# Kernel optimization log

Measured on AMD Instinct MI355X. Metric: run time of the kernel, lower is better.

## Reference

```python
import jax, jax.numpy as jnp
import numpy as np

B, D, C = 16384, 2048, 1000  # batch, in_features (feature dim), out_features (classes)
INIT_SCALE = 10.0
EPS = 1e-12


def setup_inputs() -> dict:
    key = jax.random.key(0)
    k1, k2 = jax.random.split(key)
    x = jax.random.normal(k1, (B, D), dtype=jnp.float32)
    weights = jax.random.normal(k2, (C, D), dtype=jnp.float32)  # prototypes
    scales = jnp.ones((1,), dtype=jnp.float32) * INIT_SCALE
    return {"x": x, "weights": weights, "scales": scales}


def reference(x, weights, scales):
    # Pairwise Euclidean distance between features [B,D] and prototypes [C,D]
    x2 = jnp.sum(x * x, axis=-1, keepdims=True)            # [B,1]
    w2 = jnp.sum(weights * weights, axis=-1)               # [C]
    cross = jnp.einsum('bd,cd->bc', x, weights)            # [B,C]
    d2 = jnp.maximum(x2 + w2[None, :] - 2.0 * cross, EPS)  # clamp for sqrt stability
    distances = jnp.sqrt(d2)                               # [B,C]
    logits = -scales * distances  # dml forward: -self.learn(distances)
    return logits
```

## Files before the change

### kernel.cpp

```cpp
#include <hip/hip_runtime.h>
#include <hip/hip_bf16.h>
#include <stdint.h>

#define B_ROWS 16384
#define D_K    2048
#define C_COLS 1000
#define C_PAD  1024
#define EPS_D2 1e-12f

typedef __attribute__((ext_vector_type(8))) short bf16x8;
typedef __attribute__((ext_vector_type(4))) float f32x4;

__device__ __forceinline__ unsigned short f2bf_rne(float f) {
    union { float f; uint32_t u; } a; a.f = f;
    uint32_t u = a.u;
    uint32_t r = (u + 0x7FFFu + ((u >> 16) & 1u)) >> 16;
    return (unsigned short)r;
}

__device__ __forceinline__ void async16(void* lds, const void* g) {
    __builtin_amdgcn_global_load_lds(
        (const __attribute__((address_space(1))) unsigned int*)g,
        (__attribute__((address_space(3))) unsigned int*)lds,
        16, 0, 0);
}

__global__ __launch_bounds__(256) void prep_kernel(
    const float* __restrict__ x, const float* __restrict__ w,
    __hip_bfloat16* __restrict__ xb, __hip_bfloat16* __restrict__ wb,
    float* __restrict__ x2, float* __restrict__ w2) {
    const int t = threadIdx.x;
    const int wave = t >> 6;
    const int lane = t & 63;
    const int row = blockIdx.x * 4 + wave;

    const float* src;
    __hip_bfloat16* dst;
    float* norm_out;
    bool valid;
    if (row < B_ROWS) {
        src = x + (size_t)row * D_K;
        dst = xb + (size_t)row * D_K;
        norm_out = x2 + row;
        valid = true;
    } else {
        int c = row - B_ROWS;
        src = w + (size_t)c * D_K;
        dst = wb + (size_t)c * D_K;
        norm_out = w2 + c;
        valid = (c < C_COLS);
    }

    float4 v[8];
    if (valid) {
        const float4* s4 = (const float4*)src;
        #pragma unroll
        for (int i = 0; i < 8; i++) v[i] = s4[lane + 64 * i];
    } else {
        #pragma unroll
        for (int i = 0; i < 8; i++) v[i] = make_float4(0.f, 0.f, 0.f, 0.f);
    }

    float ss = 0.f;
    uint2* d2p = (uint2*)dst;
    #pragma unroll
    for (int i = 0; i < 8; i++) {
        ss += v[i].x * v[i].x + v[i].y * v[i].y + v[i].z * v[i].z + v[i].w * v[i].w;
        uint2 p;
        p.x = (uint32_t)f2bf_rne(v[i].x) | ((uint32_t)f2bf_rne(v[i].y) << 16);
        p.y = (uint32_t)f2bf_rne(v[i].z) | ((uint32_t)f2bf_rne(v[i].w) << 16);
        d2p[lane + 64 * i] = p;
    }

    #pragma unroll
    for (int off = 32; off > 0; off >>= 1) ss += __shfl_down(ss, off, 64);
    if (lane == 0 && valid) *norm_out = ss;
}

__global__ __launch_bounds__(256) void dml_gemm(
    const __hip_bfloat16* __restrict__ A,
    const __hip_bfloat16* __restrict__ Bm,
    const float* __restrict__ x2, const float* __restrict__ w2,
    const float* __restrict__ scales, float* __restrict__ out)
{
    __shared__ __align__(16) __hip_bfloat16 lsA[128 * 32];
    __shared__ __align__(16) __hip_bfloat16 lsB[128 * 32];

    const int tid  = threadIdx.x;
    const int wave = tid >> 6;
    const int lane = tid & 63;

    const int id  = blockIdx.y * 8 + blockIdx.x;
    const int xcd = id & 7;
    const int j   = id >> 3;
    const int m0  = (xcd * 16 + (j >> 3)) * 128;
    const int n0  = (j & 7) * 128;

    const int wm = wave >> 1;
    const int wn = wave & 1;

    const int srow = wave * 32 + (lane >> 2);
    const int slot = lane & 3;
    const int ssw  = (srow >> 1) & 3;
    const int scol = (slot ^ ssw) * 8;
    const __hip_bfloat16* gA0 = A  + (size_t)(m0 + srow) * D_K + scol;
    const __hip_bfloat16* gA1 = gA0 + (size_t)16 * D_K;
    const __hip_bfloat16* gB0 = Bm + (size_t)(n0 + srow) * D_K + scol;
    const __hip_bfloat16* gB1 = gB0 + (size_t)16 * D_K;
    char* lA0 = (char*)lsA + wave * 32 * 64 + lane * 16;
    char* lA1 = lA0 + 16 * 64;
    char* lB0 = (char*)lsB + wave * 32 * 64 + lane * 16;
    char* lB1 = lB0 + 16 * 64;

    const int fr  = lane & 15;
    const int fq  = lane >> 4;
    const int fsw = (fr >> 1) & 3;
    const __hip_bfloat16* fA = lsA + (wm * 64 + fr) * 32 + (fq ^ fsw) * 8;
    const __hip_bfloat16* fB = lsB + (wn * 64 + fr) * 32 + (fq ^ fsw) * 8;

    f32x4 acc[4][4] = {};

    for (int k0 = 0; k0 < D_K; k0 += 32) {
        __syncthreads();
        async16(lA0, gA0); async16(lA1, gA1);
        async16(lB0, gB0); async16(lB1, gB1);
        gA0 += 32; gA1 += 32; gB0 += 32; gB1 += 32;
        __syncthreads();

        bf16x8 a[4], b[4];
        #pragma unroll
        for (int i = 0; i < 4; i++) a[i] = *(const bf16x8*)(fA + i * 16 * 32);
        #pragma unroll
        for (int j2 = 0; j2 < 4; j2++) b[j2] = *(const bf16x8*)(fB + j2 * 16 * 32);
        #pragma unroll
        for (int i = 0; i < 4; i++)
            #pragma unroll
            for (int j2 = 0; j2 < 4; j2++)
                acc[i][j2] = __builtin_amdgcn_mfma_f32_16x16x32_bf16(a[i], b[j2], acc[i][j2], 0, 0, 0);
    }

    const float s = scales[0];
    const int colb = n0 + wn * 64 + fr;
    const int rowb = m0 + wm * 64 + fq * 4;

    float xv[4][4];
    #pragma unroll
    for (int i = 0; i < 4; i++)
        #pragma unroll
        for (int r = 0; r < 4; r++)
            xv[i][r] = x2[rowb + i * 16 + r];

    #pragma unroll
    for (int j2 = 0; j2 < 4; j2++) {
        const int gn = colb + j2 * 16;
        const bool nok = (gn < C_COLS);
        const float w2v = nok ? w2[gn] : 0.f;
        #pragma unroll
        for (int i = 0; i < 4; i++) {
            const int gm = rowb + i * 16;
            #pragma unroll
            for (int r = 0; r < 4; r++) {
                float d2 = xv[i][r] + w2v - 2.0f * acc[i][j2][r];
                d2 = fmaxf(d2, EPS_D2);
                float val = -s * __builtin_sqrtf(d2);
                if (nok) out[(size_t)(gm + r) * C_COLS + gn] = val;
            }
        }
    }
}

extern "C" void kernel_launch(void* const* d_in, const int* in_sizes, int n_in,
                              void* d_out, int out_size, void* d_ws, size_t ws_size,
                              hipStream_t stream) {
    const float* x      = (const float*)d_in[0];
    const float* w      = (const float*)d_in[1];
    const float* scales = (const float*)d_in[2];
    float* out = (float*)d_out;

    char* ws = (char*)d_ws;
    __hip_bfloat16* xb = (__hip_bfloat16*)ws;
    __hip_bfloat16* wb = (__hip_bfloat16*)(ws + (size_t)B_ROWS * D_K * 2);
    float* x2 = (float*)(ws + (size_t)B_ROWS * D_K * 2 + (size_t)C_PAD * D_K * 2);
    float* w2 = x2 + B_ROWS;

    prep_kernel<<<dim3((B_ROWS + C_PAD) / 4), dim3(256), 0, stream>>>(x, w, xb, wb, x2, w2);
    dml_gemm<<<dim3(8, B_ROWS / 128), dim3(256), 0, stream>>>(xb, wb, x2, w2, scales, out);
}
```

Measured before the change: 320.1 us.

## Fuse x bf16 conversion and norm into GEMM, double-buffer B, stage output via LDS

The x prep pass is removed. The GEMM now loads fp32 x tiles directly, converts them to bf16 into LDS and accumulates row squared norms in-kernel, which avoids writing and re-reading a bf16 copy of x. The W tile is double-buffered with async loads overlapping compute, and the epilogue stages results in LDS so stores go out as coalesced float4 rows. The cost is that each of the 8 column blocks re-reads and re-converts the fp32 x rows, doubling A-tile global traffic per block, and the epilogue adds extra barriers.

```diff
diff --git a/kernel.cpp b/kernel.cpp
--- a/kernel.cpp
+++ b/kernel.cpp
@@ -11,13 +11,6 @@
 typedef __attribute__((ext_vector_type(8))) short bf16x8;
 typedef __attribute__((ext_vector_type(4))) float f32x4;
 
-__device__ __forceinline__ unsigned short f2bf_rne(float f) {
-    union { float f; uint32_t u; } a; a.f = f;
-    uint32_t u = a.u;
-    uint32_t r = (u + 0x7FFFu + ((u >> 16) & 1u)) >> 16;
-    return (unsigned short)r;
-}
-
 __device__ __forceinline__ void async16(void* lds, const void* g) {
     __builtin_amdgcn_global_load_lds(
         (const __attribute__((address_space(1))) unsigned int*)g,
@@ -25,31 +18,23 @@
         16, 0, 0);
 }
 
-__global__ __launch_bounds__(256) void prep_kernel(
-    const float* __restrict__ x, const float* __restrict__ w,
-    __hip_bfloat16* __restrict__ xb, __hip_bfloat16* __restrict__ wb,
-    float* __restrict__ x2, float* __restrict__ w2) {
+__device__ __forceinline__ uint2 pack_bf16x4(float4 v) {
+    union { __hip_bfloat162 h; uint32_t u; } a, b;
+    a.h = __float22bfloat162_rn(make_float2(v.x, v.y));
+    b.h = __float22bfloat162_rn(make_float2(v.z, v.w));
+    uint2 r; r.x = a.u; r.y = b.u; return r;
+}
+
+__global__ __launch_bounds__(256) void wprep(
+    const float* __restrict__ w, __hip_bfloat16* __restrict__ wb, float* __restrict__ w2) {
     const int t = threadIdx.x;
     const int wave = t >> 6;
     const int lane = t & 63;
     const int row = blockIdx.x * 4 + wave;
-
-    const float* src;
-    __hip_bfloat16* dst;
-    float* norm_out;
-    bool valid;
-    if (row < B_ROWS) {
-        src = x + (size_t)row * D_K;
-        dst = xb + (size_t)row * D_K;
-        norm_out = x2 + row;
-        valid = true;
-    } else {
-        int c = row - B_ROWS;
-        src = w + (size_t)c * D_K;
-        dst = wb + (size_t)c * D_K;
-        norm_out = w2 + c;
-        valid = (c < C_COLS);
-    }
+    const bool valid = (row < C_COLS);
+
+    const float* src = w + (size_t)row * D_K;
+    uint2* dst = (uint2*)(wb + (size_t)row * D_K);
 
     float4 v[8];
     if (valid) {
@@ -60,31 +45,28 @@
         #pragma unroll
         for (int i = 0; i < 8; i++) v[i] = make_float4(0.f, 0.f, 0.f, 0.f);
     }
-
     float ss = 0.f;
-    uint2* d2p = (uint2*)dst;
     #pragma unroll
     for (int i = 0; i < 8; i++) {
         ss += v[i].x * v[i].x + v[i].y * v[i].y + v[i].z * v[i].z + v[i].w * v[i].w;
-        uint2 p;
-        p.x = (uint32_t)f2bf_rne(v[i].x) | ((uint32_t)f2bf_rne(v[i].y) << 16);
-        p.y = (uint32_t)f2bf_rne(v[i].z) | ((uint32_t)f2bf_rne(v[i].w) << 16);
-        d2p[lane + 64 * i] = p;
-    }
-
+        dst[lane + 64 * i] = pack_bf16x4(v[i]);
+    }
     #pragma unroll
     for (int off = 32; off > 0; off >>= 1) ss += __shfl_down(ss, off, 64);
-    if (lane == 0 && valid) *norm_out = ss;
-}
-
-__global__ __launch_bounds__(256) void dml_gemm(
-    const __hip_bfloat16* __restrict__ A,
-    const __hip_bfloat16* __restrict__ Bm,
-    const float* __restrict__ x2, const float* __restrict__ w2,
+    if (lane == 0) w2[row] = valid ? ss : 0.f;
+}
+
+__global__ __launch_bounds__(256) void dml_fused(
+    const float* __restrict__ X,
+    const __hip_bfloat16* __restrict__ Wb,
+    const float* __restrict__ w2,
     const float* __restrict__ scales, float* __restrict__ out)
 {
-    __shared__ __align__(16) __hip_bfloat16 lsA[128 * 32];
-    __shared__ __align__(16) __hip_bfloat16 lsB[128 * 32];
+    __shared__ __align__(16) char smem[8192 + 2 * 8192];
+    __hip_bfloat16* lsA = (__hip_bfloat16*)smem;
+    __hip_bfloat16* lsB = (__hip_bfloat16*)(smem + 8192);
+    float* lsC = (float*)smem;
+    __shared__ float sx2[128];
 
     const int tid  = threadIdx.x;
     const int wave = tid >> 6;
@@ -96,42 +78,62 @@
     const int m0  = (xcd * 16 + (j >> 3)) * 128;
     const int n0  = (j & 7) * 128;
 
-    const int wm = wave >> 1;
-    const int wn = wave & 1;
+    const int wm = wave >> 1, wn = wave & 1;
+
+    const int rA = tid >> 3;
+    const int cA = tid & 7;
+    const float* gA = X + (size_t)(m0 + rA) * D_K + cA * 4;
+    char* lAw = (char*)lsA + rA * 64 + (((cA >> 1) ^ ((rA >> 1) & 3)) * 16) + (cA & 1) * 8;
 
     const int srow = wave * 32 + (lane >> 2);
     const int slot = lane & 3;
-    const int ssw  = (srow >> 1) & 3;
-    const int scol = (slot ^ ssw) * 8;
-    const __hip_bfloat16* gA0 = A  + (size_t)(m0 + srow) * D_K + scol;
-    const __hip_bfloat16* gA1 = gA0 + (size_t)16 * D_K;
-    const __hip_bfloat16* gB0 = Bm + (size_t)(n0 + srow) * D_K + scol;
+    const int scol = (slot ^ ((srow >> 1) & 3)) * 8;
+    const __hip_bfloat16* gB0 = Wb + (size_t)(n0 + srow) * D_K + scol;
     const __hip_bfloat16* gB1 = gB0 + (size_t)16 * D_K;
-    char* lA0 = (char*)lsA + wave * 32 * 64 + lane * 16;
-    char* lA1 = lA0 + 16 * 64;
-    char* lB0 = (char*)lsB + wave * 32 * 64 + lane * 16;
-    char* lB1 = lB0 + 16 * 64;
-
-    const int fr  = lane & 15;
-    const int fq  = lane >> 4;
+    const int lBoff = wave * 32 * 64 + lane * 16;
+
+    const int fr = lane & 15, fq = lane >> 4;
     const int fsw = (fr >> 1) & 3;
     const __hip_bfloat16* fA = lsA + (wm * 64 + fr) * 32 + (fq ^ fsw) * 8;
-    const __hip_bfloat16* fB = lsB + (wn * 64 + fr) * 32 + (fq ^ fsw) * 8;
+    const int fBoff = (wn * 64 + fr) * 32 + (fq ^ fsw) * 8;
 
     f32x4 acc[4][4] = {};
-
-    for (int k0 = 0; k0 < D_K; k0 += 32) {
-        __syncthreads();
-        async16(lA0, gA0); async16(lA1, gA1);
-        async16(lB0, gB0); async16(lB1, gB1);
-        gA0 += 32; gA1 += 32; gB0 += 32; gB1 += 32;
-        __syncthreads();
-
+    float ss[4] = {0.f, 0.f, 0.f, 0.f};
+
+    float4 vA[4];
+    #pragma unroll
+    for (int i = 0; i < 4; i++) vA[i] = *(const float4*)(gA + (size_t)i * 32 * D_K);
+    async16((char*)lsB + lBoff, gB0);
+    async16((char*)lsB + lBoff + 16 * 64, gB1);
+
+    for (int k = 0; k < 64; k++) {
+        const int buf = k & 1;
+        __syncthreads();
+
+        #pragma unroll
+        for (int i = 0; i < 4; i++) {
+            float4 v = vA[i];
+            ss[i] += v.x * v.x + v.y * v.y + v.z * v.z + v.w * v.w;
+            *(uint2*)(lAw + i * 2048) = pack_bf16x4(v);
+        }
+        __syncthreads();
+
+        if (k < 63) {
+            const float* gAn = gA + (k + 1) * 32;
+            #pragma unroll
+            for (int i = 0; i < 4; i++) vA[i] = *(const float4*)(gAn + (size_t)i * 32 * D_K);
+            const char* src0 = (const char*)(gB0 + (k + 1) * 32);
+            const char* src1 = (const char*)(gB1 + (k + 1) * 32);
+            async16((char*)lsB + (buf ^ 1) * 8192 + lBoff, src0);
+            async16((char*)lsB + (buf ^ 1) * 8192 + lBoff + 16 * 64, src1);
+        }
+
+        const __hip_bfloat16* fBb = lsB + buf * 4096 + fBoff;
         bf16x8 a[4], b[4];
         #pragma unroll
         for (int i = 0; i < 4; i++) a[i] = *(const bf16x8*)(fA + i * 16 * 32);
         #pragma unroll
-        for (int j2 = 0; j2 < 4; j2++) b[j2] = *(const bf16x8*)(fB + j2 * 16 * 32);
+        for (int j2 = 0; j2 < 4; j2++) b[j2] = *(const bf16x8*)(fBb + j2 * 16 * 32);
         #pragma unroll
         for (int i = 0; i < 4; i++)
             #pragma unroll
@@ -139,33 +141,56 @@
                 acc[i][j2] = __builtin_amdgcn_mfma_f32_16x16x32_bf16(a[i], b[j2], acc[i][j2], 0, 0, 0);
     }
 
+    #pragma unroll
+    for (int i = 0; i < 4; i++) {
+        float v = ss[i];
+        v += __shfl_down(v, 4, 8);
+        v += __shfl_down(v, 2, 8);
+        v += __shfl_down(v, 1, 8);
+        ss[i] = v;
+    }
+    if (cA == 0) {
+        sx2[rA] = ss[0]; sx2[rA + 32] = ss[1]; sx2[rA + 64] = ss[2]; sx2[rA + 96] = ss[3];
+    }
+    __syncthreads();
+
     const float s = scales[0];
-    const int colb = n0 + wn * 64 + fr;
-    const int rowb = m0 + wm * 64 + fq * 4;
-
-    float xv[4][4];
+    const int colb = wn * 64 + fr;
+    const int rowlb = wm * 64 + fq * 4;
+    float w2v[4];
+    #pragma unroll
+    for (int j2 = 0; j2 < 4; j2++) w2v[j2] = w2[n0 + colb + j2 * 16];
+    float x2v[4][4];
     #pragma unroll
     for (int i = 0; i < 4; i++)
         #pragma unroll
-        for (int r = 0; r < 4; r++)
-            xv[i][r] = x2[rowb + i * 16 + r];
-
-    #pragma unroll
-    for (int j2 = 0; j2 < 4; j2++) {
-        const int gn = colb + j2 * 16;
-        const bool nok = (gn < C_COLS);
-        const float w2v = nok ? w2[gn] : 0.f;
-        #pragma unroll
-        for (int i = 0; i < 4; i++) {
-            const int gm = rowb + i * 16;
+        for (int r = 0; r < 4; r++) x2v[i][r] = sx2[rowlb + i * 16 + r];
+
+    const int rr = tid >> 3;
+    const int gmb = m0 + (rr & 15) + (rr >> 4) * 64;
+    #pragma unroll
+    for (int i = 0; i < 4; i++) {
+        #pragma unroll
+        for (int j2 = 0; j2 < 4; j2++)
             #pragma unroll
             for (int r = 0; r < 4; r++) {
-                float d2 = xv[i][r] + w2v - 2.0f * acc[i][j2][r];
+                float d2 = x2v[i][r] + w2v[j2] - 2.0f * acc[i][j2][r];
                 d2 = fmaxf(d2, EPS_D2);
-                float val = -s * __builtin_sqrtf(d2);
-                if (nok) out[(size_t)(gm + r) * C_COLS + gn] = val;
+                lsC[(wm * 16 + fq * 4 + r) * 132 + colb + j2 * 16] = -s * __builtin_sqrtf(d2);
+            }
+        __syncthreads();
+        {
+            float* orow = out + (size_t)(gmb + i * 16) * C_COLS + n0;
+            #pragma unroll
+            for (int q = 0; q < 4; q++) {
+                const int f = (tid & 7) + 8 * q;
+                if ((n0 >> 2) + f < C_COLS / 4) {
+                    float4 val = *(const float4*)(lsC + rr * 132 + f * 4);
+                    *(float4*)(orow + f * 4) = val;
+                }
             }
         }
+        __syncthreads();
     }
 }
 
@@ -178,11 +203,9 @@
     float* out = (float*)d_out;
 
     char* ws = (char*)d_ws;
-    __hip_bfloat16* xb = (__hip_bfloat16*)ws;
-    __hip_bfloat16* wb = (__hip_bfloat16*)(ws + (size_t)B_ROWS * D_K * 2);
-    float* x2 = (float*)(ws + (size_t)B_ROWS * D_K * 2 + (size_t)C_PAD * D_K * 2);
-    float* w2 = x2 + B_ROWS;
-
-    prep_kernel<<<dim3((B_ROWS + C_PAD) / 4), dim3(256), 0, stream>>>(x, w, xb, wb, x2, w2);
-    dml_gemm<<<dim3(8, B_ROWS / 128), dim3(256), 0, stream>>>(xb, wb, x2, w2, scales, out);
-}
+    __hip_bfloat16* wb = (__hip_bfloat16*)ws;
+    float* w2 = (float*)(ws + (size_t)C_PAD * D_K * 2);
+
+    wprep<<<dim3(C_PAD / 4), dim3(256), 0, stream>>>(w, wb, w2);
+    dml_fused<<<dim3(8, B_ROWS / 128), dim3(256), 0, stream>>>(x, wb, w2, scales, out);
+}
```

After: 379.5 us. +18.5%, slower.
